# Optimization experiments

Measured on AMD Instinct MI355X. Metric: run time of the kernel, lower is better.

The kernel has to match this reference:

```python
import jax, jax.numpy as jnp
import numpy as np

N_ROIS = 10000
N_CLS = 151          # Visual Genome: 150 object classes + background
NMS_THRESH = 0.3     # filter_det default
SCORE_THRESH = 0.05  # ObjectDetector thresh
MAX_PER_IMG = 64     # ObjectDetector max_per_img
PRE_NMS_TOPN = 6000  # filter_det default
POST_NMS_TOPN = 300  # filter_det default


def setup_inputs() -> dict:
    key = jax.random.key(0)
    k1, k2, k3, k4, k5 = jax.random.split(key, 5)
    # class-probability-like scores (rows sum to 1, like the softmax output fed to filter_det)
    scores = jax.nn.softmax(jax.random.normal(k1, (N_ROIS, N_CLS)) * 2.0, axis=1)
    cx = jax.random.uniform(k2, (N_ROIS, N_CLS)) * 992.0
    cy = jax.random.uniform(k3, (N_ROIS, N_CLS)) * 992.0
    w = 4.0 + jax.random.uniform(k4, (N_ROIS, N_CLS)) * 156.0
    h = 4.0 + jax.random.uniform(k5, (N_ROIS, N_CLS)) * 156.0
    boxes = jnp.clip(jnp.stack([cx - w / 2, cy - h / 2, cx + w / 2, cy + h / 2], axis=-1), 0.0, 1023.0)
    return {"scores": scores.astype(jnp.float32), "boxes": boxes.astype(jnp.float32)}


def _nms_keep(scores_c, boxes_c):
    """apply_nms for one class: fixed-iteration greedy NMS -> bool keep mask [N]."""
    n = scores_c.shape[0]
    # pre_nms_topn: only the top-K scoring boxes are NMS candidates
    kth = jax.lax.top_k(scores_c, PRE_NMS_TOPN)[0][-1]
    active0 = scores_c >= kth
    keep0 = jnp.zeros((n,), dtype=bool)
    areas = (boxes_c[:, 2] - boxes_c[:, 0] + 1.0) * (boxes_c[:, 3] - boxes_c[:, 1] + 1.0)

    def step(carry, _):
        active, keep = carry
        s = jnp.where(active, scores_c, -jnp.inf)
        idx = jnp.argmax(s)
        valid = s[idx] > -jnp.inf  # any candidate left?
        keep = keep.at[idx].set(keep[idx] | valid)
        b = boxes_c[idx]
        ix1 = jnp.maximum(b[0], boxes_c[:, 0])
        iy1 = jnp.maximum(b[1], boxes_c[:, 1])
        ix2 = jnp.minimum(b[2], boxes_c[:, 2])
        iy2 = jnp.minimum(b[3], boxes_c[:, 3])
        inter = jnp.maximum(ix2 - ix1 + 1.0, 0.0) * jnp.maximum(iy2 - iy1 + 1.0, 0.0)
        iou = inter / (areas[idx] + areas - inter)
        # suppress iou > thresh (self box has iou 1, so it is removed too)
        active = active & (iou <= NMS_THRESH)
        return (active, keep), None

    (_, keep), _ = jax.lax.scan(step, (active0, keep0), None, length=POST_NMS_TOPN)
    return keep


def reference(scores, boxes):
    """filter_det: per-class NMS mask + cross-class dedupe + top max_per_img."""
    # per-class NMS, vmapped over the class axis -> keep mask [N, C]
    keep = jax.vmap(_nms_keep, in_axes=(1, 1), out_axes=1)(scores, boxes)
    keep = jax.lax.stop_gradient(keep)  # mask built from .data in the original
    # valid_cls: skip background (col 0) and classes whose best score <= thresh
    col_valid = (jnp.max(scores, axis=0) > SCORE_THRESH).at[0].set(False)
    nms_mask = keep & col_valid[None, :]
    dists_all = jnp.where(nms_mask, scores, 0.0)  # nms_mask * scores
    # nms_filter_duplicates: one label per box (argmax over classes)
    scores_pre = jnp.max(dists_all, axis=1)
    labels_pre = jnp.argmax(dists_all, axis=1)
    # sort descending, threshold, cap at max_per_img (fixed-shape top_k + validity mask)
    s_masked = jnp.where(scores_pre > SCORE_THRESH, scores_pre, -jnp.inf)
    top_v, top_i = jax.lax.top_k(s_masked, MAX_PER_IMG)
    valid = top_v > SCORE_THRESH
    top_scores = jnp.where(valid, top_v, 0.0)
    top_labels = jnp.where(valid, labels_pre[top_i], -1)
    top_inds = jnp.where(valid, top_i, -1)
    return dists_all, top_scores, top_inds, top_labels
```

## Files before the change

kernel.cpp:

```cpp
#include <hip/hip_runtime.h>

typedef unsigned long long u64;
typedef unsigned int u32;

#define N_ROIS   10000
#define N_CLS    151
#define PRE_TOPN 6000
#define POST_TOPN 300
#define MAX_PER  64
#define NMS_TH   0.3f
#define SCORE_TH 0.05f

#define BLOCKA   1024
#define NWAVES   (BLOCKA / 64)
#define BANDK    512
#define BANDCAP  1024
#define CHUNK    640
#define CWORDS   (CHUNK / 32)
#define TROWS    10240

#define KEYS_OFF  40000
#define RNK_OFF   48192
#define SBOX_OFF  52288
#define SIDX_OFF  68672
#define SUPP_OFF  72768
#define KBOX_OFF  123968
#define SMEM_BYTES 128832

__device__ __forceinline__ bool suppresses(float4 a, float4 b)
{
#pragma clang fp contract(off)
    float areaa = (a.z - a.x + 1.f) * (a.w - a.y + 1.f);
    float areab = (b.z - b.x + 1.f) * (b.w - b.y + 1.f);
    float ix1 = fmaxf(a.x, b.x), iy1 = fmaxf(a.y, b.y);
    float ix2 = fminf(a.z, b.z), iy2 = fminf(a.w, b.w);
    float iw = fmaxf(ix2 - ix1 + 1.f, 0.f);
    float ih = fmaxf(iy2 - iy1 + 1.f, 0.f);
    float inter = iw * ih;
    float iou = inter / (areaa + areab - inter);
    return iou > NMS_TH;
}

__global__ __launch_bounds__(BLOCKA)
void nms_kernel(const float* __restrict__ scores,
                const float* __restrict__ scoresT,
                const float* __restrict__ boxes,
                float* __restrict__ dists,
                u64* __restrict__ rowkey,
                int useT)
{
    extern __shared__ __align__(16) char smem[];
    __shared__ int s_cnts[32];
    __shared__ int s_cc, s_nk;
    __shared__ u32 s_redu[NWAVES];
    __shared__ u32 s_alive[CWORDS], s_rz[CWORDS];
    __shared__ int s_wpre[CWORDS];
    __shared__ int s_wofs[NWAVES + 1];
    __shared__ int s_resume;

    u32*    sbits = (u32*)smem;
    u64*    keys  = (u64*)(smem + KEYS_OFF);
    u32*    rnk   = (u32*)(smem + RNK_OFF);
    float4* sbox  = (float4*)(smem + SBOX_OFF);
    u32*    sidx  = (u32*)(smem + SIDX_OFF);
    u32*    supp  = (u32*)(smem + SUPP_OFF);
    float4* kbox  = (float4*)(smem + KBOX_OFF);

    const int c    = blockIdx.x + 1;
    const int tid  = threadIdx.x;
    const int lane = tid & 63, wid = tid >> 6;

    u32 lmax = 0;
    if (useT) {
        const float* colp = scoresT + (size_t)c * TROWS;
        for (int r = tid; r < N_ROIS; r += BLOCKA) {
            u32 b = __float_as_uint(colp[r]); sbits[r] = b; lmax = b > lmax ? b : lmax;
        }
    } else {
        for (int r = tid; r < N_ROIS; r += BLOCKA) {
            u32 b = __float_as_uint(scores[(size_t)r * N_CLS + c]); sbits[r] = b; lmax = b > lmax ? b : lmax;
        }
    }
    for (int off = 32; off; off >>= 1) { u32 o = __shfl_down(lmax, off); lmax = o > lmax ? o : lmax; }
    if (lane == 0) s_redu[wid] = lmax;
    if (tid < 32) s_cnts[tid] = 0;
    __syncthreads();
    if (tid == 0) {
        u32 m = s_redu[0];
        for (int w = 1; w < NWAVES; ++w) m = s_redu[w] > m ? s_redu[w] : m;
        s_redu[0] = m; s_nk = 0;
    }
    __syncthreads();
    if (s_redu[0] <= __float_as_uint(SCORE_TH)) return;

    int slot = 0;
    auto count_ge = [&](u32 v) -> int {
        int cnt = 0;
        const u64* sb2 = (const u64*)sbits;
        for (int r2 = tid; r2 < N_ROIS / 2; r2 += BLOCKA) {
            u64 two = sb2[r2];
            cnt += ((u32)two >= v) ? 1 : 0;
            cnt += ((u32)(two >> 32) >= v) ? 1 : 0;
        }
        for (int off = 32; off; off >>= 1) cnt += __shfl_down(cnt, off);
        if (lane == 0 && cnt) atomicAdd(&s_cnts[slot & 31], cnt);
        __syncthreads();
        int total = s_cnts[slot & 31];
        if (tid == 0) s_cnts[(slot + 16) & 31] = 0;
        ++slot;
        return total;
    };

    auto compactRange = [&](u32 vlo, u32 vhiX, int pos0) -> int {
        if (tid == 0) s_cc = 0;
        __syncthreads();
        for (int r = tid; r < TROWS; r += BLOCKA) {
            bool pred = (r < N_ROIS) && (sbits[r] >= vlo) && (sbits[r] < vhiX);
            u64 ball = __ballot(pred);
            int bpos = 0, bcnt = __popcll(ball);
            if (lane == 0 && bcnt) bpos = atomicAdd(&s_cc, bcnt);
            bpos = __shfl(bpos, 0);
            if (pred) {
                int pos = pos0 + bpos + (int)__popcll(ball & ((1ull << lane) - 1ull));
                if (pos < BANDCAP)
                    keys[pos] = ((u64)sbits[r] << 32) | (u64)(0xFFFFFFFFu - (u32)r);
            }
        }
        __syncthreads();
        return s_cc;
    };

    auto emitEq = [&](u32 v, int rowStart, int pos0, int capN, int* emittedOut) -> int {
        int run = 0, resume = N_ROIS;
        for (int r0 = 0; r0 < N_ROIS; r0 += BLOCKA) {
            if (r0 + BLOCKA <= rowStart) continue;
            int r = r0 + tid;
            bool pred = (r < N_ROIS) && (r >= rowStart) && (sbits[r] == v);
            u64 ball = __ballot(pred);
            if (lane == 0) s_wofs[wid] = __popcll(ball);
            __syncthreads();
            if (tid == 0) {
                int acc = 0;
                for (int w = 0; w < NWAVES; ++w) { int cw = s_wofs[w]; s_wofs[w] = acc; acc += cw; }
                s_wofs[NWAVES] = acc; s_resume = N_ROIS;
            }
            __syncthreads();
            int tot = s_wofs[NWAVES];
            if (pred) {
                int idx = run + s_wofs[wid] + (int)__popcll(ball & ((1ull << lane) - 1ull));
                if (idx < capN) keys[pos0 + idx] = ((u64)v << 32) | (u64)(0xFFFFFFFFu - (u32)r);
                else atomicMin(&s_resume, r);
            }
            __syncthreads();
            if (run + tot > capN) {
                resume = s_resume < (r0 + BLOCKA) ? s_resume : (r0 + BLOCKA);
                run = capN;
                break;
            }
            run += tot;
        }
        *emittedOut = run;
        return resume;
    };

    u32 Vhi = 0x80000000u;
    int procCnt = 0, knum = 0;
    u32 Vfloor = 0; int eligTotal = 0x7FFFFFFF; bool haveFloor = false;
    u32 eqV = 0; int eqRow = N_ROIS; bool eqPend = false;

    for (int band = 0; band < 64 && knum < POST_TOPN; ++band) {
        int C = 0;
        if (eqPend) {
            int E; int resume = emitEq(eqV, eqRow, 0, BANDCAP, &E);
            C = E; procCnt += E;
            if (resume >= N_ROIS) { eqPend = false; Vhi = eqV; }
            eqRow = resume;
            if (C == 0) { if (eqPend) break; else continue; }
        } else {
            if (band >= 1) {
                if (!haveFloor) {
                    u32 V = 0; int cv = N_ROIS;
                    for (int b = 30; b >= 0; --b) {
                        u32 cd = V | (1u << b);
                        int c2 = count_ge(cd);
                        if (c2 >= PRE_TOPN) { V = cd; cv = c2; }
                    }
                    Vfloor = V; eligTotal = cv; haveFloor = true;
                }
                if (procCnt >= eligTotal) break;
            }
            int target = procCnt + BANDK;
            int capAbs = procCnt + BANDCAP;
            u32 V = 0; int cv = N_ROIS;
            for (int b = 30; b >= 16; --b) {
                u32 cd = V | (1u << b);
                int c2 = count_ge(cd);
                if (c2 >= target) { V = cd; cv = c2; }
            }
            for (int b = 15; b >= 0 && cv > capAbs; --b) {
                u32 cd = V | (1u << b);
                int c2 = count_ge(cd);
                if (c2 >= target) { V = cd; cv = c2; }
            }
            if (haveFloor && V < Vfloor) { V = Vfloor; cv = eligTotal; }
            if (cv > capAbs) {
                int ngt = compactRange(V + 1, Vhi, 0);
                int E; int resume = emitEq(V, 0, ngt, BANDCAP - ngt, &E);
                C = ngt + E; procCnt += C;
                eqV = V; eqRow = resume; eqPend = (resume < N_ROIS);
                if (!eqPend) Vhi = V;
            } else {
                C = compactRange(V, Vhi, 0);
                procCnt = cv; Vhi = V;
            }
            if (C <= 0) continue;
        }

        for (int q = tid; q < BANDCAP; q += BLOCKA) rnk[q] = 0;
        __syncthreads();
        {
            int q0 = tid >> 1, par = tid & 1;
            for (int q = q0; q < C; q += BLOCKA / 2) {
                u64 kq = keys[q]; int partial = 0;
                for (int p = par; p < C; p += 2) partial += (keys[p] > kq) ? 1 : 0;
                atomicAdd(&rnk[q], (u32)partial);
            }
        }
        __syncthreads();
        for (int q = tid; q < C; q += BLOCKA) {
            u64 kq = keys[q];
            u32 pos = rnk[q];
            u32 r = 0xFFFFFFFFu - (u32)kq;
            sidx[pos] = r;
            sbox[pos] = *(const float4*)(boxes + ((size_t)r * N_CLS + c) * 4);
        }
        __syncthreads();

        for (int base = 0; base < C && knum < POST_TOPN; base += CHUNK) {
            int chunkN = (C - base) < CHUNK ? (C - base) : CHUNK;
            int knum0 = knum;

            if (tid < CHUNK) {
                bool al = false;
                if (tid < chunkN) {
                    al = true;
                    float4 bq = sbox[base + tid];
                    for (int j = 0; j < knum0; ++j)
                        if (suppresses(kbox[j], bq)) { al = false; break; }
                }
                u64 ball = __ballot(al);
                if (lane == 0) { s_alive[wid * 2] = (u32)ball; s_alive[wid * 2 + 1] = (u32)(ball >> 32); }
            }
            if (tid < CWORDS) s_rz[tid] = 0;
            for (int w = tid; w < CHUNK * CWORDS; w += BLOCKA) supp[w] = 0;
            __syncthreads();

            {
                int q0 = tid >> 1, par = tid & 1;
                for (int q = q0; q < chunkN; q += BLOCKA / 2) {
                    if (!((s_alive[q >> 5] >> (q & 31)) & 1u)) continue;
                    float4 bq = sbox[base + q];
                    for (int p = par; p < q; p += 2) {
                        if (!((s_alive[p >> 5] >> (p & 31)) & 1u)) continue;
                        if (suppresses(sbox[base + p], bq)) {
                            atomicOr(&supp[p * CWORDS + (q >> 5)], 1u << (q & 31));
                            atomicOr(&s_rz[p >> 5], 1u << (p & 31));
                        }
                    }
                }
            }
            __syncthreads();

            if (wid == 0) {
                u32 aw  = (lane < CWORDS) ? s_alive[lane] : 0u;
                u32 rzw = (lane < CWORDS) ? s_rz[lane] : 0u;
                const int budget = POST_TOPN - knum0;
                int truncTo = -1;
                while (true) {
                    u32 pz = aw & rzw;
                    u64 bal = __ballot(pz != 0u);
                    if (!bal) break;
                    int pl = __ffsll(bal) - 1;
                    u32 wv = __shfl(pz, pl);
                    int b = __ffs(wv) - 1;
                    int p = (pl << 5) + b;
                    int cb = (lane < pl) ? __popc(aw) : ((lane == pl) ? __popc(aw & ((1u << b) - 1u)) : 0);
                    for (int off = 32; off; off >>= 1) cb += __shfl_down(cb, off);
                    int before = __shfl(cb, 0);
                    if (before >= budget) { truncTo = budget; break; }
                    int widx = (lane < CWORDS) ? lane : 0;
                    u32 row = supp[p * CWORDS + widx];
                    if (lane < CWORDS) aw &= ~row;
                    if (lane == pl) { aw |= (1u << b); rzw &= ~(1u << b); }
                    if (before + 1 >= budget) { truncTo = budget; break; }
                }
                if (truncTo < 0) {
                    int pcT = __popc(aw);
                    for (int off = 32; off; off >>= 1) pcT += __shfl_down(pcT, off);
                    if (__shfl(pcT, 0) > budget) truncTo = budget;
                }
                if (truncTo >= 0) {
                    int pcf = __popc(aw);
                    int inc = pcf;
                    for (int off = 1; off < 64; off <<= 1) { int o = __shfl_up(inc, off); if (lane >= off) inc += o; }
                    int ex = inc - pcf;
                    int need = truncTo - ex;
                    if (need <= 0) aw = 0;
                    else if (need < pcf) {
                        while (__popc(aw) > need) aw &= ~(1u << (31 - __clz(aw)));
                    }
                }
                if (lane < CWORDS) s_alive[lane] = aw;
                int pcf2 = __popc(aw);
                int inc2 = pcf2;
                for (int off = 1; off < 64; off <<= 1) { int o = __shfl_up(inc2, off); if (lane >= off) inc2 += o; }
                if (lane < CWORDS) s_wpre[lane] = inc2 - pcf2;
                int totF = __shfl(inc2, 63);
                if (lane == 0) s_nk = knum0 + totF;
            }
            __syncthreads();

            if (tid < CHUNK) {
                int w = tid >> 5, b = tid & 31;
                u32 word = s_alive[w];
                if ((word >> b) & 1u) {
                    int rank = knum0 + s_wpre[w] + __popc(word & ((1u << b) - 1u));
                    int q = base + tid;
                    u32 r = sidx[q];
                    u32 sb = sbits[r];
                    kbox[rank] = sbox[q];
                    dists[(size_t)r * N_CLS + c] = __uint_as_float(sb);
                    atomicMax(rowkey + r, ((u64)sb << 32) | (u64)(0xFFFFFFFFu - (u32)c));
                }
            }
            __syncthreads();
            knum = s_nk;
        }
    }
}

__global__ __launch_bounds__(1024)
void transpose_zero_kernel(const float* __restrict__ in, float* __restrict__ outT,
                           float* __restrict__ dists, u64* __restrict__ rowkey, int useT)
{
    __shared__ float tile[32][33];
    if (useT) {
        int tx = threadIdx.x & 31, ty = threadIdx.x >> 5;
        int rb = blockIdx.x * 32, cb = blockIdx.y * 32;
        int r = rb + ty, cc = cb + tx;
        tile[ty][tx] = (r < N_ROIS && cc < N_CLS) ? in[(size_t)r * N_CLS + cc] : 0.f;
        __syncthreads();
        int oc = cb + ty, orr = rb + tx;
        if (oc < N_CLS) outT[(size_t)oc * TROWS + orr] = tile[tx][ty];
    }
    int bid = blockIdx.y * gridDim.x + blockIdx.x;
    int flat = bid * 1024 + threadIdx.x;
    if (flat < N_ROIS * N_CLS) dists[flat] = 0.f;
    if (flat < N_ROIS) rowkey[flat] = 0ull;
}

__global__ __launch_bounds__(BLOCKA)
void topk_kernel(const u64* __restrict__ rowkey, float* __restrict__ out)
{
    __shared__ u32 shi[N_ROIS];
    __shared__ int s_cnts[32];
    __shared__ int s_cc;
    __shared__ u64 cand[192];
    __shared__ int s_wofs[NWAVES + 1];
    const int tid = threadIdx.x, lane = tid & 63, wid = tid >> 6;

    if (tid < 32) s_cnts[tid] = 0;
    if (tid == 0) s_cc = 0;
    if (tid < 192) cand[tid] = 0;
    for (int i = tid; i < N_ROIS; i += BLOCKA) {
        u64 rk = rowkey[i];
        u32 hb = (u32)(rk >> 32);
        shi[i] = (__uint_as_float(hb) > SCORE_TH) ? hb : 0u;
    }
    __syncthreads();

    int slot = 0;
    auto count_ge = [&](u32 v) -> int {
        int cnt = 0;
        const u64* s2 = (const u64*)shi;
        for (int r2 = tid; r2 < N_ROIS / 2; r2 += BLOCKA) {
            u64 two = s2[r2];
            cnt += ((u32)two >= v) ? 1 : 0;
            cnt += ((u32)(two >> 32) >= v) ? 1 : 0;
        }
        for (int off = 32; off; off >>= 1) cnt += __shfl_down(cnt, off);
        if (lane == 0 && cnt) atomicAdd(&s_cnts[slot & 31], cnt);
        __syncthreads();
        int total = s_cnts[slot & 31];
        if (tid == 0) s_cnts[(slot + 16) & 31] = 0;
        ++slot;
        return total;
    };

    const int cap = 128;
    u32 V = 0; int cv = N_ROIS;
    for (int b = 30; b >= 16; --b) {
        u32 cd = V | (1u << b);
        int c2 = count_ge(cd);
        if (c2 >= MAX_PER) { V = cd; cv = c2; }
    }
    for (int b = 15; b >= 0 && cv > cap; --b) {
        u32 cd = V | (1u << b);
        int c2 = count_ge(cd);
        if (c2 >= MAX_PER) { V = cd; cv = c2; }
    }
    if (V == 0) { V = 1; cv = count_ge(1); }
    int C = 0;
    if (cv > cap) {
        if (tid == 0) s_cc = 0;
        __syncthreads();
        for (int i = tid; i < TROWS; i += BLOCKA) {
            bool pred = (i < N_ROIS) && (shi[i] >= V + 1);
            u64 ball = __ballot(pred);
            int bpos = 0, bcnt = __popcll(ball);
            if (lane == 0 && bcnt) bpos = atomicAdd(&s_cc, bcnt);
            bpos = __shfl(bpos, 0);
            if (pred) {
                int pos = bpos + (int)__popcll(ball & ((1ull << lane) - 1ull));
                if (pos < cap) cand[pos] = ((u64)shi[i] << 32) | (u64)(0xFFFFFFFFu - (u32)i);
            }
        }
        __syncthreads();
        int ngt = s_cc; if (ngt > cap) ngt = cap;
        int need = MAX_PER - ngt;
        int run = 0;
        for (int r0 = 0; r0 < N_ROIS && run < need; r0 += BLOCKA) {
            int r = r0 + tid;
            bool pred = (r < N_ROIS) && (shi[r] == V);
            u64 ball = __ballot(pred);
            if (lane == 0) s_wofs[wid] = __popcll(ball);
            __syncthreads();
            if (tid == 0) {
                int acc = 0;
                for (int w = 0; w < NWAVES; ++w) { int cw = s_wofs[w]; s_wofs[w] = acc; acc += cw; }
                s_wofs[NWAVES] = acc;
            }
            __syncthreads();
            int tot = s_wofs[NWAVES];
            if (pred) {
                int idx = run + s_wofs[wid] + (int)__popcll(ball & ((1ull << lane) - 1ull));
                if (idx < need) cand[ngt + idx] = ((u64)V << 32) | (u64)(0xFFFFFFFFu - (u32)r);
            }
            __syncthreads();
            run += tot;
        }
        C = ngt + (run < need ? run : need);
    } else {
        if (tid == 0) s_cc = 0;
        __syncthreads();
        for (int i = tid; i < TROWS; i += BLOCKA) {
            bool pred = (i < N_ROIS) && (shi[i] >= V);
            u64 ball = __ballot(pred);
            int bpos = 0, bcnt = __popcll(ball);
            if (lane == 0 && bcnt) bpos = atomicAdd(&s_cc, bcnt);
            bpos = __shfl(bpos, 0);
            if (pred) {
                int pos = bpos + (int)__popcll(ball & ((1ull << lane) - 1ull));
                if (pos < cap) cand[pos] = ((u64)shi[i] << 32) | (u64)(0xFFFFFFFFu - (u32)i);
            }
        }
        __syncthreads();
        C = s_cc; if (C > cap) C = cap;
    }

    float* out_s = out + (size_t)N_ROIS * N_CLS;
    float* out_i = out_s + MAX_PER;
    float* out_l = out_i + MAX_PER;

    int myrank = -1; u64 myk = 0;
    if (tid < C) {
        myk = cand[tid];
        myrank = 0;
        for (int p = 0; p < C; ++p) myrank += (cand[p] > myk) ? 1 : 0;
    }
    if (tid < MAX_PER) { out_s[tid] = 0.f; out_i[tid] = -1.f; out_l[tid] = -1.f; }
    __syncthreads();
    if (tid < C && myrank < MAX_PER) {
        u32 r = 0xFFFFFFFFu - (u32)myk;
        out_s[myrank] = __uint_as_float((u32)(myk >> 32));
        out_i[myrank] = (float)r;
        out_l[myrank] = (float)(0xFFFFFFFFu - (u32)rowkey[r]);
    }
}

extern "C" void kernel_launch(void* const* d_in, const int* in_sizes, int n_in,
                              void* d_out, int out_size, void* d_ws, size_t ws_size,
                              hipStream_t stream)
{
    const float* scores = (const float*)d_in[0];
    const float* boxes  = (const float*)d_in[1];
    float* out = (float*)d_out;
    u64* rowkey = (u64*)d_ws;

    size_t needT = 80000 + (size_t)N_CLS * TROWS * sizeof(float);
    int useT = (ws_size >= needT) ? 1 : 0;
    float* scoresT = (float*)((char*)d_ws + 80000);

    (void)hipFuncSetAttribute((const void*)nms_kernel,
                              hipFuncAttributeMaxDynamicSharedMemorySize, SMEM_BYTES);

    transpose_zero_kernel<<<dim3(320, 5), 1024, 0, stream>>>(scores, scoresT, out, rowkey, useT);
    nms_kernel<<<N_CLS - 1, BLOCKA, SMEM_BYTES, stream>>>(scores, scoresT, boxes, out, rowkey, useT);
    topk_kernel<<<1, BLOCKA, 0, stream>>>(rowkey, out);
}
```

Measured before the change: 249.4 us.

## Replace serial wave-0 chunk NMS resolve with block-parallel fixed-point iteration

Each chunk's greedy resolve no longer runs as a serial loop in a single wave. The whole block now repeatedly ORs the suppression rows of currently-kept suppressors and recomputes the kept mask until it stops changing. The chunk size shrinks to 512 so that one box pair maps to two threads without an outer loop, while the band parameters (BANDK, BANDCAP) grow and the shared-memory layout is rearranged to fit. The cost is several block-wide barriers per fixed-point iteration and possibly more chunks overall.

```diff
diff --git a/kernel.cpp b/kernel.cpp
--- a/kernel.cpp
+++ b/kernel.cpp
@@ -13,19 +13,20 @@
 
 #define BLOCKA   1024
 #define NWAVES   (BLOCKA / 64)
-#define BANDK    512
-#define BANDCAP  1024
-#define CHUNK    640
+#define BANDK    1024
+#define BANDCAP  1536
+#define CHUNK    512
 #define CWORDS   (CHUNK / 32)
 #define TROWS    10240
 
+#define SBITS_OFF 0
 #define KEYS_OFF  40000
-#define RNK_OFF   48192
-#define SBOX_OFF  52288
-#define SIDX_OFF  68672
-#define SUPP_OFF  72768
-#define KBOX_OFF  123968
-#define SMEM_BYTES 128832
+#define RNK_OFF   52288
+#define SBOX_OFF  58432
+#define SIDX_OFF  83008
+#define SUPP_OFF  89152
+#define KBOX_OFF  121920
+#define SMEM_BYTES 126784
 
 __device__ __forceinline__ bool suppresses(float4 a, float4 b)
 {
@@ -51,9 +52,10 @@
 {
     extern __shared__ __align__(16) char smem[];
     __shared__ int s_cnts[32];
-    __shared__ int s_cc, s_nk;
+    __shared__ int s_cc, s_nk, s_chg;
     __shared__ u32 s_redu[NWAVES];
     __shared__ u32 s_alive[CWORDS], s_rz[CWORDS];
+    __shared__ u32 s_K[CWORDS], s_Supp[CWORDS];
     __shared__ int s_wpre[CWORDS];
     __shared__ int s_wofs[NWAVES + 1];
     __shared__ int s_resume;
@@ -257,72 +259,69 @@
 
             {
                 int q0 = tid >> 1, par = tid & 1;
-                for (int q = q0; q < chunkN; q += BLOCKA / 2) {
-                    if (!((s_alive[q >> 5] >> (q & 31)) & 1u)) continue;
-                    float4 bq = sbox[base + q];
-                    for (int p = par; p < q; p += 2) {
+                if (q0 < chunkN && ((s_alive[q0 >> 5] >> (q0 & 31)) & 1u)) {
+                    float4 bq = sbox[base + q0];
+                    for (int p = par; p < q0; p += 2) {
                         if (!((s_alive[p >> 5] >> (p & 31)) & 1u)) continue;
                         if (suppresses(sbox[base + p], bq)) {
-                            atomicOr(&supp[p * CWORDS + (q >> 5)], 1u << (q & 31));
+                            atomicOr(&supp[(p << 4) + (q0 >> 5)], 1u << (q0 & 31));
                             atomicOr(&s_rz[p >> 5], 1u << (p & 31));
                         }
                     }
                 }
             }
-            __syncthreads();
+            if (tid < CWORDS) s_K[tid] = 0;
+            __syncthreads();
+
+            if (tid < CWORDS) s_K[tid] = s_alive[tid];
+            for (;;) {
+                __syncthreads();
+                if (tid < CWORDS) s_Supp[tid] = 0;
+                if (tid == 0) s_chg = 0;
+                __syncthreads();
+                for (int pw = tid; pw < (chunkN << 4); pw += BLOCKA) {
+                    int p = pw >> 4, w = pw & 15;
+                    if (((s_rz[p >> 5] >> (p & 31)) & 1u) &&
+                        ((s_K[p >> 5] >> (p & 31)) & 1u)) {
+                        u32 rw = supp[(p << 4) + w];
+                        if (rw) atomicOr(&s_Supp[w], rw);
+                    }
+                }
+                __syncthreads();
+                if (tid < CWORDS) {
+                    u32 nk = s_alive[tid] & ~s_Supp[tid];
+                    if (nk != s_K[tid]) { s_K[tid] = nk; atomicOr(&s_chg, 1); }
+                }
+                __syncthreads();
+                if (!s_chg) break;
+            }
 
             if (wid == 0) {
-                u32 aw  = (lane < CWORDS) ? s_alive[lane] : 0u;
-                u32 rzw = (lane < CWORDS) ? s_rz[lane] : 0u;
-                const int budget = POST_TOPN - knum0;
-                int truncTo = -1;
-                while (true) {
-                    u32 pz = aw & rzw;
-                    u64 bal = __ballot(pz != 0u);
-                    if (!bal) break;
-                    int pl = __ffsll(bal) - 1;
-                    u32 wv = __shfl(pz, pl);
-                    int b = __ffs(wv) - 1;
-                    int p = (pl << 5) + b;
-                    int cb = (lane < pl) ? __popc(aw) : ((lane == pl) ? __popc(aw & ((1u << b) - 1u)) : 0);
-                    for (int off = 32; off; off >>= 1) cb += __shfl_down(cb, off);
-                    int before = __shfl(cb, 0);
-                    if (before >= budget) { truncTo = budget; break; }
-                    int widx = (lane < CWORDS) ? lane : 0;
-                    u32 row = supp[p * CWORDS + widx];
-                    if (lane < CWORDS) aw &= ~row;
-                    if (lane == pl) { aw |= (1u << b); rzw &= ~(1u << b); }
-                    if (before + 1 >= budget) { truncTo = budget; break; }
-                }
-                if (truncTo < 0) {
-                    int pcT = __popc(aw);
-                    for (int off = 32; off; off >>= 1) pcT += __shfl_down(pcT, off);
-                    if (__shfl(pcT, 0) > budget) truncTo = budget;
-                }
-                if (truncTo >= 0) {
-                    int pcf = __popc(aw);
-                    int inc = pcf;
-                    for (int off = 1; off < 64; off <<= 1) { int o = __shfl_up(inc, off); if (lane >= off) inc += o; }
-                    int ex = inc - pcf;
-                    int need = truncTo - ex;
-                    if (need <= 0) aw = 0;
-                    else if (need < pcf) {
-                        while (__popc(aw) > need) aw &= ~(1u << (31 - __clz(aw)));
+                u32 kw = (lane < CWORDS) ? s_K[lane] : 0u;
+                int pc = __popc(kw);
+                int inc = pc;
+                for (int off = 1; off < 32; off <<= 1) { int o = __shfl_up(inc, off); if (lane >= off) inc += o; }
+                int ex = inc - pc;
+                int budget = POST_TOPN - knum0;
+                u32 fin = kw;
+                if (ex >= budget) fin = 0;
+                else {
+                    int need = budget - ex;
+                    if (pc > need) {
+                        while (__popc(fin) > need) fin &= ~(1u << (31 - __clz(fin)));
                     }
                 }
-                if (lane < CWORDS) s_alive[lane] = aw;
-                int pcf2 = __popc(aw);
-                int inc2 = pcf2;
-                for (int off = 1; off < 64; off <<= 1) { int o = __shfl_up(inc2, off); if (lane >= off) inc2 += o; }
-                if (lane < CWORDS) s_wpre[lane] = inc2 - pcf2;
-                int totF = __shfl(inc2, 63);
-                if (lane == 0) s_nk = knum0 + totF;
+                int pc2 = __popc(fin);
+                int inc2 = pc2;
+                for (int off = 1; off < 32; off <<= 1) { int o = __shfl_up(inc2, off); if (lane >= off) inc2 += o; }
+                if (lane < CWORDS) { s_K[lane] = fin; s_wpre[lane] = inc2 - pc2; }
+                if (lane == CWORDS - 1) s_nk = knum0 + inc2;
             }
             __syncthreads();
 
             if (tid < CHUNK) {
                 int w = tid >> 5, b = tid & 31;
-                u32 word = s_alive[w];
+                u32 word = s_K[w];
                 if ((word >> b) & 1u) {
                     int rank = knum0 + s_wpre[w] + __popc(word & ((1u << b) - 1u));
                     int q = base + tid;
```

Result: slower. 259.2 us (+3.9%).
